# Optimization experiments

Hardware: AMD Instinct MI355X
Metric: run time of the kernel (lower is better)

## Reference

```python
import jax, jax.numpy as jnp
import numpy as np

N = 100000      # nodes
E = 800000      # edges (avg degree 8)
D_IN = 128      # in_channels
HEADS = 8
C = 16          # out_channels per head (heads*C = 128 output dim)
NEG_SLOPE = 0.2  # PyG GATConv default leaky_relu slope


def setup_inputs() -> dict:
    key = jax.random.key(0)
    ks = jax.random.split(key, 12)
    s = 1.0 / np.sqrt(D_IN)
    x = jax.random.normal(ks[0], (N, D_IN), jnp.float32)
    ei = jax.random.randint(ks[1], (2, E), 0, N, jnp.int32)
    return {
        "x": x,
        "ei": ei,
        # conv_in GATConv params
        "W_in": jax.random.normal(ks[2], (D_IN, HEADS * C), jnp.float32) * s,
        "a_src_in": jax.random.normal(ks[3], (HEADS, C), jnp.float32) * s,
        "a_dst_in": jax.random.normal(ks[4], (HEADS, C), jnp.float32) * s,
        "b_in": jnp.zeros((HEADS * C,), jnp.float32),
        # conv_out GATConv params (applied to flipped edges)
        "W_out": jax.random.normal(ks[5], (D_IN, HEADS * C), jnp.float32) * s,
        "a_src_out": jax.random.normal(ks[6], (HEADS, C), jnp.float32) * s,
        "a_dst_out": jax.random.normal(ks[7], (HEADS, C), jnp.float32) * s,
        "b_out": jnp.zeros((HEADS * C,), jnp.float32),
    }


def _gat_conv(x, src, dst, W, a_src, a_dst, b):
    # h: [N, H, C] projected node features
    h = (x @ W).reshape(N, HEADS, C)
    # per-node attention logits [N, H]
    alpha_src = jnp.einsum("nhc,hc->nh", h, a_src)
    alpha_dst = jnp.einsum("nhc,hc->nh", h, a_dst)
    # per-edge logits, message flows src -> dst; softmax grouped by dst
    logits = jax.nn.leaky_relu(alpha_src[src] + alpha_dst[dst], NEG_SLOPE)  # [E, H]
    seg_max = jax.ops.segment_max(logits, dst, num_segments=N)              # [N, H]
    ex = jnp.exp(logits - seg_max[dst])
    denom = jax.ops.segment_sum(ex, dst, num_segments=N)                    # [N, H]
    coef = ex / denom[dst]                                                  # [E, H]
    msg = h[src] * coef[:, :, None]                                         # [E, H, C]
    out = jax.ops.segment_sum(msg, dst, num_segments=N)                     # [N, H, C]
    return out.reshape(N, HEADS * C) + b


def reference(x, ei, W_in, a_src_in, a_dst_in, b_in, W_out, a_src_out, a_dst_out, b_out):
    src, dst = ei[0], ei[1]
    # DirSeq: conv_in on (src->dst), conv_out on flipped edges (dst->src)
    x_in = _gat_conv(x, src, dst, W_in, a_src_in, a_dst_in, b_in)
    x_out = _gat_conv(x, dst, src, W_out, a_src_out, a_dst_out, b_out)
    return x_in + x_out
```

## Files before the change

### kernel.cpp

```cpp
#include <hip/hip_runtime.h>

#define N_NODES 100000
#define N_EDGES 800000
#define NEG 0.2f
#define PB_SHIFT 8
#define PB_NODES 256
#define N_PBKT ((N_NODES + PB_NODES - 1) / PB_NODES)
#define TILE_E 4096
#define EPT 16

typedef __attribute__((ext_vector_type(8))) short bf16x8;
typedef __attribute__((ext_vector_type(4))) float f32x4;

__device__ inline unsigned short f2bf(float f) {
    unsigned u = __float_as_uint(f);
    u += 0x7fffu + ((u >> 16) & 1u);
    return (unsigned short)(u >> 16);
}
__device__ inline float bf2f_lo(unsigned u) { return __uint_as_float(u << 16); }
__device__ inline float bf2f_hi(unsigned u) { return __uint_as_float(u & 0xffff0000u); }

__global__ __launch_bounds__(256) void prep_x_kernel(
    const float* __restrict__ x, unsigned short* __restrict__ x_bf)
{
    const int i = (blockIdx.x * 256 + threadIdx.x) * 4;
    if (i >= N_NODES * 128) return;
    const float4 v = *(const float4*)&x[i];
    ushort4 o;
    o.x = f2bf(v.x); o.y = f2bf(v.y); o.z = f2bf(v.z); o.w = f2bf(v.w);
    *(ushort4*)&x_bf[i] = o;
}

__global__ __launch_bounds__(256) void prep_w_kernel(
    const float* __restrict__ W_in, const float* __restrict__ W_out,
    const float* __restrict__ as_in, const float* __restrict__ ad_in,
    const float* __restrict__ as_out, const float* __restrict__ ad_out,
    unsigned short* __restrict__ Wf, int* __restrict__ bcnt)
{
    const int t = blockIdx.x * 256 + threadIdx.x;
    if (t < 2 * N_PBKT) bcnt[t] = 0;
    if (t >= 2 * 4 * 9 * 64) return;
    const int lane = t & 63;
    const int rest = t >> 6;
    const int ct  = rest % 9;
    const int kb  = (rest / 9) & 3;
    const int dir = rest / 36;
    const float* W  = dir ? W_out  : W_in;
    const float* as = dir ? as_out : as_in;
    const float* ad = dir ? ad_out : ad_in;
    const int m16 = lane & 15, quad = lane >> 4;

    bf16x8 o;
#pragma unroll
    for (int j = 0; j < 8; ++j) {
        const int k = kb * 32 + quad * 8 + j;
        float v;
        if (ct < 8) {
            v = W[k * 128 + ct * 16 + m16];
        } else {
            const float* av = (m16 < 8) ? as : ad;
            const int hh = m16 & 7;
            v = 0.f;
            for (int c = 0; c < 16; ++c)
                v += W[k * 128 + hh * 16 + c] * av[hh * 16 + c];
        }
        o[j] = (short)f2bf(v);
    }
    *(bf16x8*)&Wf[(long long)t * 8] = o;
}

__global__ __launch_bounds__(256) void gemm_kernel(
    const unsigned short* __restrict__ x_bf,
    const unsigned short* __restrict__ Wf,
    unsigned short* __restrict__ h_in, unsigned short* __restrict__ h_out,
    float* __restrict__ asrc_in, float* __restrict__ adst_in,
    float* __restrict__ asrc_out, float* __restrict__ adst_out)
{
    const int dir = blockIdx.y;
    unsigned short* h = dir ? h_out : h_in;
    float* asrc = dir ? asrc_out : asrc_in;
    float* adst = dir ? adst_out : adst_in;

    const int tid  = threadIdx.x;
    const int lane = tid & 63;
    const int wave = tid >> 6;
    const int m16  = lane & 15;
    const int quad = lane >> 4;
    const int rbase = blockIdx.x * 128 + wave * 32;

    f32x4 acc[2][8];
    f32x4 acc_a[2];
#pragma unroll
    for (int rt = 0; rt < 2; ++rt) {
        acc_a[rt] = f32x4{0.f, 0.f, 0.f, 0.f};
#pragma unroll
        for (int ct = 0; ct < 8; ++ct)
            acc[rt][ct] = f32x4{0.f, 0.f, 0.f, 0.f};
    }

    const unsigned short* wf = Wf + (long long)dir * 4 * 9 * 64 * 8;

#pragma unroll
    for (int kb = 0; kb < 4; ++kb) {
        const int k0 = kb * 32 + quad * 8;
        bf16x8 a[2];
#pragma unroll
        for (int rt = 0; rt < 2; ++rt) {
            int r = rbase + rt * 16 + m16;
            r = r < N_NODES ? r : N_NODES - 1;
            a[rt] = *(const bf16x8*)&x_bf[(long long)r * 128 + k0];
        }
#pragma unroll
        for (int ct = 0; ct < 9; ++ct) {
            const bf16x8 b = *(const bf16x8*)&wf[(long long)((kb * 9 + ct) * 64 + lane) * 8];
            if (ct < 8) {
                acc[0][ct] = __builtin_amdgcn_mfma_f32_16x16x32_bf16(a[0], b, acc[0][ct], 0, 0, 0);
                acc[1][ct] = __builtin_amdgcn_mfma_f32_16x16x32_bf16(a[1], b, acc[1][ct], 0, 0, 0);
            } else {
                acc_a[0] = __builtin_amdgcn_mfma_f32_16x16x32_bf16(a[0], b, acc_a[0], 0, 0, 0);
                acc_a[1] = __builtin_amdgcn_mfma_f32_16x16x32_bf16(a[1], b, acc_a[1], 0, 0, 0);
            }
        }
    }

#pragma unroll
    for (int rt = 0; rt < 2; ++rt) {
#pragma unroll
        for (int r = 0; r < 4; ++r) {
            const int row = rbase + rt * 16 + quad * 4 + r;
            if (row < N_NODES) {
                unsigned short* hp = &h[(long long)row * 128 + m16];
#pragma unroll
                for (int ct = 0; ct < 8; ++ct)
                    hp[ct * 16] = f2bf(acc[rt][ct][r]);
                const float av = acc_a[rt][r];
                if (m16 < 8) asrc[row * 8 + m16] = av;
                else         adst[row * 8 + (m16 - 8)] = av;
            }
        }
    }
}

__global__ __launch_bounds__(256) void bucket_hist_kernel(
    const int* __restrict__ ei, int* __restrict__ bcnt)
{
    __shared__ int bh[2 * N_PBKT];
    const int tid = threadIdx.x;
    for (int i = tid; i < 2 * N_PBKT; i += 256) bh[i] = 0;
    __syncthreads();
    for (int e = blockIdx.x * 256 + tid; e < N_EDGES; e += gridDim.x * 256) {
        const int s = ei[e];
        const int t = ei[N_EDGES + e];
        atomicAdd(&bh[t >> PB_SHIFT], 1);
        atomicAdd(&bh[N_PBKT + (s >> PB_SHIFT)], 1);
    }
    __syncthreads();
    for (int i = tid; i < 2 * N_PBKT; i += 256) {
        const int v = bh[i];
        if (v) atomicAdd(&bcnt[i], v);
    }
}

__global__ __launch_bounds__(512) void bucket_scan_kernel(
    const int* __restrict__ bcnt,
    int* __restrict__ boffs0, int* __restrict__ boffs1,
    int* __restrict__ gcur,
    int* __restrict__ offs_in, int* __restrict__ offs_out)
{
    const int dir = blockIdx.x;
    const int* c = bcnt + dir * N_PBKT;
    int* bo = dir ? boffs1 : boffs0;
    int* gc = gcur + dir * N_PBKT;

    __shared__ int sm[512];
    const int tid = threadIdx.x;
    const int v = (tid < N_PBKT) ? c[tid] : 0;
    sm[tid] = v;
    __syncthreads();
#pragma unroll
    for (int off = 1; off < 512; off <<= 1) {
        int t = (tid >= off) ? sm[tid - off] : 0;
        __syncthreads();
        sm[tid] += t;
        __syncthreads();
    }
    if (tid < N_PBKT) {
        const int excl = sm[tid] - v;
        bo[tid] = excl;
        gc[tid] = excl;
    }
    if (tid == N_PBKT - 1) bo[N_PBKT] = sm[tid];
    if (tid == 0) (dir ? offs_out : offs_in)[N_NODES] = N_EDGES;
}

__global__ __launch_bounds__(256) void partition_kernel(
    const int* __restrict__ ei, int* __restrict__ gcur,
    int* __restrict__ binned0, int* __restrict__ binned1)
{
    const int dir = blockIdx.y;
    int* binned = dir ? binned1 : binned0;
    int* gc = gcur + dir * N_PBKT;

    __shared__ int hist[N_PBKT];
    __shared__ int curs[N_PBKT];
    const int tid = threadIdx.x;
    for (int i = tid; i < N_PBKT; i += 256) hist[i] = 0;
    __syncthreads();

    const int e0 = blockIdx.x * TILE_E;
    int key[EPT], val[EPT];
#pragma unroll
    for (int i = 0; i < EPT; ++i) {
        const int e = e0 + i * 256 + tid;
        if (e < N_EDGES) {
            const int s = ei[e];
            const int t = ei[N_EDGES + e];
            key[i] = dir ? s : t;
            val[i] = dir ? t : s;
            atomicAdd(&hist[key[i] >> PB_SHIFT], 1);
        } else {
            key[i] = -1; val[i] = 0;
        }
    }
    __syncthreads();
    for (int b = tid; b < N_PBKT; b += 256) {
        const int c = hist[b];
        curs[b] = c ? atomicAdd(&gc[b], c) : 0;
    }
    __syncthreads();
#pragma unroll
    for (int i = 0; i < EPT; ++i) {
        if (key[i] >= 0) {
            const int pos = atomicAdd(&curs[key[i] >> PB_SHIFT], 1);
            binned[pos] = (val[i] << 8) | (key[i] & (PB_NODES - 1));
        }
    }
}

__global__ __launch_bounds__(256) void place_kernel(
    const int* __restrict__ binned0, const int* __restrict__ binned1,
    const int* __restrict__ boffs0, const int* __restrict__ boffs1,
    int* __restrict__ adj_in, int* __restrict__ adj_out,
    int* __restrict__ offs_in, int* __restrict__ offs_out)
{
    const int b   = blockIdx.x;
    const int dir = blockIdx.y;
    const int* bp = dir ? binned1 : binned0;
    const int* bo = dir ? boffs1  : boffs0;
    int* adj  = dir ? adj_out  : adj_in;
    int* offs = dir ? offs_out : offs_in;

    const int base = b << PB_SHIFT;
    const int beg = bo[b], end = bo[b + 1];
    const int tid = threadIdx.x;

    __shared__ int cnt[PB_NODES];
    __shared__ int sc[PB_NODES];
    __shared__ int cur[PB_NODES];

    cnt[tid] = 0;
    __syncthreads();
    for (int p = beg + tid; p < end; p += 256)
        atomicAdd(&cnt[bp[p] & (PB_NODES - 1)], 1);
    __syncthreads();
    const int v = cnt[tid];
    sc[tid] = v;
    __syncthreads();
#pragma unroll
    for (int off = 1; off < PB_NODES; off <<= 1) {
        int t = (tid >= off) ? sc[tid - off] : 0;
        __syncthreads();
        sc[tid] += t;
        __syncthreads();
    }
    const int excl = beg + sc[tid] - v;
    cur[tid] = excl;
    const int node = base + tid;
    if (node < N_NODES) offs[node] = excl;
    __syncthreads();
    for (int p = beg + tid; p < end; p += 256) {
        const int pk = bp[p];
        adj[atomicAdd(&cur[pk & (PB_NODES - 1)], 1)] = pk >> 8;
    }
}

__global__ __launch_bounds__(256) void gather_kernel(
    const int* __restrict__ offs_in, const int* __restrict__ adj_in,
    const int* __restrict__ offs_out, const int* __restrict__ adj_out,
    const unsigned short* __restrict__ h_in, const unsigned short* __restrict__ h_out,
    const float* __restrict__ asrc_in, const float* __restrict__ adst_in,
    const float* __restrict__ asrc_out, const float* __restrict__ adst_out,
    const float* __restrict__ b_in, const float* __restrict__ b_out,
    float* __restrict__ out)
{
    const int n = (blockIdx.x * 256 + threadIdx.x) >> 6;
    if (n >= N_NODES) return;
    const int lane = threadIdx.x & 63;
    const int c0 = lane * 2;
    const int hh = lane >> 3;

    float acc0 = b_in[c0] + b_out[c0];
    float acc1 = b_in[c0 + 1] + b_out[c0 + 1];

#define DIR_BLOCK(OFFS, ADJ, HX, ASRC, ADST)                                   \
    {                                                                          \
        const int beg = OFFS[n], end = OFFS[n + 1];                            \
        if (end > beg) {                                                       \
            const float ad = ADST[n * 8 + hh];                                 \
            float num0 = 0.f, num1 = 0.f, den = 0.f;                           \
            int p = beg;                                                       \
            for (; p + 4 <= end; p += 4) {                                     \
                const int nb0 = ADJ[p], nb1 = ADJ[p + 1];                      \
                const int nb2 = ADJ[p + 2], nb3 = ADJ[p + 3];                  \
                const float s0 = ASRC[nb0 * 8 + hh], s1 = ASRC[nb1 * 8 + hh];  \
                const float s2 = ASRC[nb2 * 8 + hh], s3 = ASRC[nb3 * 8 + hh];  \
                const unsigned v0 = *(const unsigned*)&HX[(long long)nb0 * 128 + c0]; \
                const unsigned v1 = *(const unsigned*)&HX[(long long)nb1 * 128 + c0]; \
                const unsigned v2 = *(const unsigned*)&HX[(long long)nb2 * 128 + c0]; \
                const unsigned v3 = *(const unsigned*)&HX[(long long)nb3 * 128 + c0]; \
                float l0 = s0 + ad; l0 = l0 > 0.f ? l0 : NEG * l0;             \
                float l1 = s1 + ad; l1 = l1 > 0.f ? l1 : NEG * l1;             \
                float l2 = s2 + ad; l2 = l2 > 0.f ? l2 : NEG * l2;             \
                float l3 = s3 + ad; l3 = l3 > 0.f ? l3 : NEG * l3;             \
                const float w0 = __expf(l0), w1 = __expf(l1);                  \
                const float w2 = __expf(l2), w3 = __expf(l3);                  \
                den += (w0 + w1) + (w2 + w3);                                  \
                num0 += w0 * bf2f_lo(v0) + w1 * bf2f_lo(v1)                    \
                      + w2 * bf2f_lo(v2) + w3 * bf2f_lo(v3);                   \
                num1 += w0 * bf2f_hi(v0) + w1 * bf2f_hi(v1)                    \
                      + w2 * bf2f_hi(v2) + w3 * bf2f_hi(v3);                   \
            }                                                                  \
            for (; p < end; ++p) {                                             \
                const int nb = ADJ[p];                                         \
                float l = ASRC[nb * 8 + hh] + ad;                              \
                l = l > 0.f ? l : NEG * l;                                     \
                const float w = __expf(l);                                     \
                den += w;                                                      \
                const unsigned hv = *(const unsigned*)&HX[(long long)nb * 128 + c0]; \
                num0 += w * bf2f_lo(hv);                                       \
                num1 += w * bf2f_hi(hv);                                       \
            }                                                                  \
            acc0 += num0 / den;                                                \
            acc1 += num1 / den;                                                \
        }                                                                      \
    }

    DIR_BLOCK(offs_in, adj_in, h_in, asrc_in, adst_in)
    DIR_BLOCK(offs_out, adj_out, h_out, asrc_out, adst_out)
#undef DIR_BLOCK

    *(float2*)&out[(long long)n * 128 + c0] = float2{acc0, acc1};
}

extern "C" void kernel_launch(void* const* d_in, const int* in_sizes, int n_in,
                              void* d_out, int out_size, void* d_ws, size_t ws_size,
                              hipStream_t stream) {
    const float* x      = (const float*)d_in[0];
    const int*   ei     = (const int*)  d_in[1];
    const float* W_in   = (const float*)d_in[2];
    const float* as_in  = (const float*)d_in[3];
    const float* ad_in  = (const float*)d_in[4];
    const float* b_in   = (const float*)d_in[5];
    const float* W_out  = (const float*)d_in[6];
    const float* as_out = (const float*)d_in[7];
    const float* ad_out = (const float*)d_in[8];
    const float* b_out  = (const float*)d_in[9];
    float* out = (float*)d_out;

    char* ws = (char*)d_ws;
    const long long NH = (long long)N_NODES * 128;
    unsigned short* x_bf  = (unsigned short*)ws;    ws += NH * 2;
    unsigned short* h_in  = (unsigned short*)ws;    ws += NH * 2;
    unsigned short* h_out = (unsigned short*)ws;    ws += NH * 2;
    unsigned short* Wf    = (unsigned short*)ws;    ws += 2LL * 4 * 9 * 64 * 8 * 2;
    float* asrc_in   = (float*)ws;                  ws += N_NODES * 8 * 4;
    float* adst_in   = (float*)ws;                  ws += N_NODES * 8 * 4;
    float* asrc_out  = (float*)ws;                  ws += N_NODES * 8 * 4;
    float* adst_out  = (float*)ws;                  ws += N_NODES * 8 * 4;
    int* binned0     = (int*)ws;                    ws += (long long)N_EDGES * 4;
    int* binned1     = (int*)ws;                    ws += (long long)N_EDGES * 4;
    int* adj_in      = (int*)ws;                    ws += N_EDGES * 4;
    int* adj_out     = (int*)ws;                    ws += N_EDGES * 4;
    int* offs_in     = (int*)ws;                    ws += (N_NODES + 1) * 4;
    int* offs_out    = (int*)ws;                    ws += (N_NODES + 1) * 4;
    int* bcnt        = (int*)ws;                    ws += 2 * N_PBKT * 4;
    int* boffs0      = (int*)ws;                    ws += (N_PBKT + 1) * 4;
    int* boffs1      = (int*)ws;                    ws += (N_PBKT + 1) * 4;
    int* gcur        = (int*)ws;                    ws += 2 * N_PBKT * 4;

    prep_x_kernel<<<(N_NODES * 128 / 4 + 255) / 256, 256, 0, stream>>>(x, x_bf);
    prep_w_kernel<<<(2 * 4 * 9 * 64 + 255) / 256, 256, 0, stream>>>(
        W_in, W_out, as_in, ad_in, as_out, ad_out, Wf, bcnt);

    dim3 gemm_grid((N_NODES + 127) / 128, 2);
    gemm_kernel<<<gemm_grid, 256, 0, stream>>>(
        x_bf, Wf, h_in, h_out, asrc_in, adst_in, asrc_out, adst_out);

    bucket_hist_kernel<<<192, 256, 0, stream>>>(ei, bcnt);
    bucket_scan_kernel<<<2, 512, 0, stream>>>(
        bcnt, boffs0, boffs1, gcur, offs_in, offs_out);
    partition_kernel<<<dim3((N_EDGES + TILE_E - 1) / TILE_E, 2), 256, 0, stream>>>(
        ei, gcur, binned0, binned1);
    place_kernel<<<dim3(N_PBKT, 2), 256, 0, stream>>>(
        binned0, binned1, boffs0, boffs1, adj_in, adj_out, offs_in, offs_out);

    gather_kernel<<<(N_NODES * 64 + 255) / 256, 256, 0, stream>>>(
        offs_in, adj_in, offs_out, adj_out, h_in, h_out,
        asrc_in, adst_in, asrc_out, adst_out, b_in, b_out, out);
}
```

Baseline: 303.7 us.

## Fuse x bf16 conversion with edge histogram and share edge weights via shuffles

```diff
diff --git a/kernel.cpp b/kernel.cpp
--- a/kernel.cpp
+++ b/kernel.cpp
@@ -8,6 +8,8 @@
 #define N_PBKT ((N_NODES + PB_NODES - 1) / PB_NODES)
 #define TILE_E 4096
 #define EPT 16
+#define PREP_BLOCKS ((N_NODES * 128 / 4 + 255) / 256)
+#define HIST_BLOCKS 192
 
 typedef __attribute__((ext_vector_type(8))) short bf16x8;
 typedef __attribute__((ext_vector_type(4))) float f32x4;
@@ -19,17 +21,6 @@
 }
 __device__ inline float bf2f_lo(unsigned u) { return __uint_as_float(u << 16); }
 __device__ inline float bf2f_hi(unsigned u) { return __uint_as_float(u & 0xffff0000u); }
-
-__global__ __launch_bounds__(256) void prep_x_kernel(
-    const float* __restrict__ x, unsigned short* __restrict__ x_bf)
-{
-    const int i = (blockIdx.x * 256 + threadIdx.x) * 4;
-    if (i >= N_NODES * 128) return;
-    const float4 v = *(const float4*)&x[i];
-    ushort4 o;
-    o.x = f2bf(v.x); o.y = f2bf(v.y); o.z = f2bf(v.z); o.w = f2bf(v.w);
-    *(ushort4*)&x_bf[i] = o;
-}
 
 __global__ __launch_bounds__(256) void prep_w_kernel(
     const float* __restrict__ W_in, const float* __restrict__ W_out,
@@ -69,6 +60,37 @@
     *(bf16x8*)&Wf[(long long)t * 8] = o;
 }
 
+__global__ __launch_bounds__(256) void prep_hist_kernel(
+    const float* __restrict__ x, unsigned short* __restrict__ x_bf,
+    const int* __restrict__ ei, int* __restrict__ bcnt)
+{
+    const int tid = threadIdx.x;
+    if (blockIdx.x < PREP_BLOCKS) {
+        const int i = (blockIdx.x * 256 + tid) * 4;
+        if (i >= N_NODES * 128) return;
+        const float4 v = *(const float4*)&x[i];
+        ushort4 o;
+        o.x = f2bf(v.x); o.y = f2bf(v.y); o.z = f2bf(v.z); o.w = f2bf(v.w);
+        *(ushort4*)&x_bf[i] = o;
+        return;
+    }
+    __shared__ int bh[2 * N_PBKT];
+    for (int i = tid; i < 2 * N_PBKT; i += 256) bh[i] = 0;
+    __syncthreads();
+    const int hb = blockIdx.x - PREP_BLOCKS;
+    for (int e = hb * 256 + tid; e < N_EDGES; e += HIST_BLOCKS * 256) {
+        const int s = ei[e];
+        const int t = ei[N_EDGES + e];
+        atomicAdd(&bh[t >> PB_SHIFT], 1);
+        atomicAdd(&bh[N_PBKT + (s >> PB_SHIFT)], 1);
+    }
+    __syncthreads();
+    for (int i = tid; i < 2 * N_PBKT; i += 256) {
+        const int v = bh[i];
+        if (v) atomicAdd(&bcnt[i], v);
+    }
+}
+
 __global__ __launch_bounds__(256) void gemm_kernel(
     const unsigned short* __restrict__ x_bf,
     const unsigned short* __restrict__ Wf,
@@ -138,26 +160,6 @@
                 else         adst[row * 8 + (m16 - 8)] = av;
             }
         }
-    }
-}
-
-__global__ __launch_bounds__(256) void bucket_hist_kernel(
-    const int* __restrict__ ei, int* __restrict__ bcnt)
-{
-    __shared__ int bh[2 * N_PBKT];
-    const int tid = threadIdx.x;
-    for (int i = tid; i < 2 * N_PBKT; i += 256) bh[i] = 0;
-    __syncthreads();
-    for (int e = blockIdx.x * 256 + tid; e < N_EDGES; e += gridDim.x * 256) {
-        const int s = ei[e];
-        const int t = ei[N_EDGES + e];
-        atomicAdd(&bh[t >> PB_SHIFT], 1);
-        atomicAdd(&bh[N_PBKT + (s >> PB_SHIFT)], 1);
-    }
-    __syncthreads();
-    for (int i = tid; i < 2 * N_PBKT; i += 256) {
-        const int v = bh[i];
-        if (v) atomicAdd(&bcnt[i], v);
     }
 }
 
@@ -298,6 +300,8 @@
     const int lane = threadIdx.x & 63;
     const int c0 = lane * 2;
     const int hh = lane >> 3;
+    const int g8 = lane & 7;
+    const int grpbase = lane & 56;
 
     float acc0 = b_in[c0] + b_out[c0];
     float acc1 = b_in[c0 + 1] + b_out[c0 + 1];
@@ -309,37 +313,43 @@
             const float ad = ADST[n * 8 + hh];                                 \
             float num0 = 0.f, num1 = 0.f, den = 0.f;                           \
             int p = beg;                                                       \
-            for (; p + 4 <= end; p += 4) {                                     \
-                const int nb0 = ADJ[p], nb1 = ADJ[p + 1];                      \
-                const int nb2 = ADJ[p + 2], nb3 = ADJ[p + 3];                  \
-                const float s0 = ASRC[nb0 * 8 + hh], s1 = ASRC[nb1 * 8 + hh];  \
-                const float s2 = ASRC[nb2 * 8 + hh], s3 = ASRC[nb3 * 8 + hh];  \
-                const unsigned v0 = *(const unsigned*)&HX[(long long)nb0 * 128 + c0]; \
-                const unsigned v1 = *(const unsigned*)&HX[(long long)nb1 * 128 + c0]; \
-                const unsigned v2 = *(const unsigned*)&HX[(long long)nb2 * 128 + c0]; \
-                const unsigned v3 = *(const unsigned*)&HX[(long long)nb3 * 128 + c0]; \
-                float l0 = s0 + ad; l0 = l0 > 0.f ? l0 : NEG * l0;             \
-                float l1 = s1 + ad; l1 = l1 > 0.f ? l1 : NEG * l1;             \
-                float l2 = s2 + ad; l2 = l2 > 0.f ? l2 : NEG * l2;             \
-                float l3 = s3 + ad; l3 = l3 > 0.f ? l3 : NEG * l3;             \
-                const float w0 = __expf(l0), w1 = __expf(l1);                  \
-                const float w2 = __expf(l2), w3 = __expf(l3);                  \
-                den += (w0 + w1) + (w2 + w3);                                  \
-                num0 += w0 * bf2f_lo(v0) + w1 * bf2f_lo(v1)                    \
-                      + w2 * bf2f_lo(v2) + w3 * bf2f_lo(v3);                   \
-                num1 += w0 * bf2f_hi(v0) + w1 * bf2f_hi(v1)                    \
-                      + w2 * bf2f_hi(v2) + w3 * bf2f_hi(v3);                   \
-            }                                                                  \
-            for (; p < end; ++p) {                                             \
-                const int nb = ADJ[p];                                         \
-                float l = ASRC[nb * 8 + hh] + ad;                              \
+            for (; p + 8 <= end; p += 8) {                                     \
+                const int nb_mine = ADJ[p + g8];                               \
+                float l = ASRC[nb_mine * 8 + hh] + ad;                         \
                 l = l > 0.f ? l : NEG * l;                                     \
                 const float w = __expf(l);                                     \
                 den += w;                                                      \
-                const unsigned hv = *(const unsigned*)&HX[(long long)nb * 128 + c0]; \
-                num0 += w * bf2f_lo(hv);                                       \
-                num1 += w * bf2f_hi(hv);                                       \
+                _Pragma("unroll")                                              \
+                for (int g = 0; g < 8; ++g) {                                  \
+                    const int   nb_g = __shfl(nb_mine, grpbase + g, 64);       \
+                    const float w_g  = __shfl(w, grpbase + g, 64);             \
+                    const unsigned hv = *(const unsigned*)&HX[(long long)nb_g * 128 + c0]; \
+                    num0 += w_g * bf2f_lo(hv);                                 \
+                    num1 += w_g * bf2f_hi(hv);                                 \
+                }                                                              \
             }                                                                  \
+            if (p < end) {                                                     \
+                const int q = p + g8;                                          \
+                const int nb_mine = (q < end) ? ADJ[q] : 0;                    \
+                float w = 0.f;                                                 \
+                if (q < end) {                                                 \
+                    float l = ASRC[nb_mine * 8 + hh] + ad;                     \
+                    l = l > 0.f ? l : NEG * l;                                 \
+                    w = __expf(l);                                             \
+                }                                                              \
+                den += w;                                                      \
+                const int cnt_t = end - p;                                     \
+                for (int g = 0; g < cnt_t; ++g) {                              \
+                    const int   nb_g = __shfl(nb_mine, grpbase + g, 64);       \
+                    const float w_g  = __shfl(w, grpbase + g, 64);             \
+                    const unsigned hv = *(const unsigned*)&HX[(long long)nb_g * 128 + c0]; \
+                    num0 += w_g * bf2f_lo(hv);                                 \
+                    num1 += w_g * bf2f_hi(hv);                                 \
+                }                                                              \
+            }                                                                  \
+            den += __shfl_xor(den, 1, 64);                                     \
+            den += __shfl_xor(den, 2, 64);                                     \
+            den += __shfl_xor(den, 4, 64);                                     \
             acc0 += num0 / den;                                                \
             acc1 += num1 / den;                                                \
         }                                                                      \
@@ -388,15 +398,15 @@
     int* boffs1      = (int*)ws;                    ws += (N_PBKT + 1) * 4;
     int* gcur        = (int*)ws;                    ws += 2 * N_PBKT * 4;
 
-    prep_x_kernel<<<(N_NODES * 128 / 4 + 255) / 256, 256, 0, stream>>>(x, x_bf);
     prep_w_kernel<<<(2 * 4 * 9 * 64 + 255) / 256, 256, 0, stream>>>(
         W_in, W_out, as_in, ad_in, as_out, ad_out, Wf, bcnt);
+    prep_hist_kernel<<<PREP_BLOCKS + HIST_BLOCKS, 256, 0, stream>>>(
+        x, x_bf, ei, bcnt);
 
     dim3 gemm_grid((N_NODES + 127) / 128, 2);
     gemm_kernel<<<gemm_grid, 256, 0, stream>>>(
         x_bf, Wf, h_in, h_out, asrc_in, adst_in, asrc_out, adst_out);
 
-    bucket_hist_kernel<<<192, 256, 0, stream>>>(ei, bcnt);
     bucket_scan_kernel<<<2, 512, 0, stream>>>(
         bcnt, boffs0, boffs1, gcur, offs_in, offs_out);
     partition_kernel<<<dim3((N_EDGES + TILE_E - 1) / TILE_E, 2), 256, 0, stream>>>(
```

Result: no change. 303.4 us (-0.1%).
